# Kernel tuning notes

Hardware: AMD Instinct MI355X
Metric: run time of the kernel (lower is better)

Reference implementation:

```python
import jax, jax.numpy as jnp
import numpy as np

IN_V = 16
OUT_V = 16
HS = 64
INCR = 2
METRIC = jnp.array([1.0, -1.0, -1.0, -1.0], dtype=jnp.float32)


def setup_inputs() -> dict:
    key = jax.random.key(0)
    ks = jax.random.split(key, 9)
    B, N = 64, 1024
    vectors = jax.random.normal(ks[0], (B, N, IN_V, 4), dtype=jnp.float32)
    scalars = jax.random.normal(ks[1], (B, N, HS), dtype=jnp.float32)
    # kaiming-uniform-ish init scale for [out, in] weights
    def w(k, o, i):
        bound = 1.0 / np.sqrt(i)
        return jax.random.uniform(k, (o, i), jnp.float32, -bound, bound)
    Wq = w(ks[2], IN_V * INCR, IN_V)
    Wk = w(ks[3], IN_V * INCR, IN_V)
    Wv = w(ks[4], OUT_V, IN_V)  # exp() applied in forward (EquiLinearTimelike)
    Wq_s = w(ks[5], HS, HS)
    Wk_s = w(ks[6], HS, HS)
    bq_s = jax.random.uniform(ks[7], (HS,), jnp.float32, -1 / np.sqrt(HS), 1 / np.sqrt(HS))
    bk_s = jax.random.uniform(ks[8], (HS,), jnp.float32, -1 / np.sqrt(HS), 1 / np.sqrt(HS))
    return {"vectors": vectors, "scalars": scalars, "Wq": Wq, "Wq_s": Wq_s,
            "bq_s": bq_s, "Wk": Wk, "Wk_s": Wk_s, "bk_s": bk_s, "Wv": Wv}


def reference(vectors, scalars, Wq, Wq_s, bq_s, Wk, Wk_s, bk_s, Wv):
    B, N = vectors.shape[:2]
    # Lorentz squared norm: t^2 - x^2 - y^2 - z^2 over last axis -> [B,N,IN_V,1]
    norm = jnp.einsum('bnik,k->bni', vectors * vectors, METRIC)[..., None]
    vecs = vectors / jnp.sqrt(jnp.clip(jnp.abs(norm), 1e-5))
    # Q/K vector projections [B,N,IN_V*INCR,4] and scalar projections [B,N,HS]
    q_v = jnp.einsum('ij,bnjk->bnik', Wq, vecs)
    k_v = jnp.einsum('ij,bnjk->bnik', Wk, vecs)
    q_s = scalars @ Wq_s.T + bq_s
    k_s = scalars @ Wk_s.T + bk_s
    # embed: flatten vectors (K gets metric factor) and concat scalars
    q = jnp.concatenate([q_v.reshape(B, N, -1), q_s], axis=-1)
    k = jnp.concatenate([(k_v * METRIC).reshape(B, N, -1), k_s], axis=-1)
    # V: positive-weight (timelike) projection, flatten -> [B,N,OUT_V*4]
    v = jnp.einsum('ij,bnjk->bnik', jnp.exp(Wv), vecs).reshape(B, N, -1)
    # scaled dot-product attention over the particle axis
    scale = 1.0 / jnp.sqrt(jnp.asarray(q.shape[-1], q.dtype))
    scores = jnp.einsum('bqd,bkd->bqk', q, k) * scale
    attn = jax.nn.softmax(scores, axis=-1)
    out = jnp.einsum('bqk,bkd->bqd', attn, v)
    return out.reshape(B, N, -1, 4)
```

## Files before the change

kernel.cpp:

```cpp
#include <hip/hip_runtime.h>
#include <math.h>

typedef float f32x16 __attribute__((ext_vector_type(16)));
typedef short bf16x8 __attribute__((ext_vector_type(8)));
typedef short bf16x4 __attribute__((ext_vector_type(4)));
typedef unsigned short u16;
typedef unsigned int u32;

#define MFMA32(a, b, c) __builtin_amdgcn_mfma_f32_32x32x16_bf16(a, b, c, 0, 0, 0)

__device__ __forceinline__ u16 f2bf(float x) {
    u32 u = __float_as_uint(x);
    u += 0x7FFFu + ((u >> 16) & 1u);
    return (u16)(u >> 16);
}
__device__ __forceinline__ float bf2f(u16 h) {
    return __uint_as_float(((u32)h) << 16);
}
__device__ __forceinline__ void gload16(const void* g, void* l) {
    __builtin_amdgcn_global_load_lds(
        (const __attribute__((address_space(1))) unsigned int*)g,
        (__attribute__((address_space(3))) unsigned int*)l, 16, 0, 0);
}

__global__ __launch_bounds__(256) void g_kernel(
    const float* __restrict__ Wq, const float* __restrict__ Wk,
    const float* __restrict__ Wv,
    u16* __restrict__ gmh, u16* __restrict__ gml,
    u16* __restrict__ mvh, u16* __restrict__ mvl)
{
    const int bk = blockIdx.x;
    const int base = ((bk & 3) * 256 + threadIdx.x) * 4;
    if (bk < 4) {
#pragma unroll
        for (int i = 0; i < 4; ++i) {
            int e = base + i;
            int f = e >> 6, fp = e & 63;
            int c = f & 3, cp = fp & 3, j = f >> 2, jp = fp >> 2;
            float val = 0.f;
            if (c == cp) {
                float a0 = 0.f, a1 = 0.f;
#pragma unroll 8
                for (int ff = 0; ff < 32; ff += 2) {
                    a0 = fmaf(Wq[ff * 16 + j],       Wk[ff * 16 + jp],       a0);
                    a1 = fmaf(Wq[(ff + 1) * 16 + j], Wk[(ff + 1) * 16 + jp], a1);
                }
                val = (a0 + a1) * ((c == 0) ? 1.f : -1.f);
            }
            u16 h = f2bf(val);
            gmh[e] = h; gml[e] = f2bf(val - bf2f(h));
        }
    } else {
#pragma unroll
        for (int i = 0; i < 4; ++i) {
            int e = base + i;
            int f = e >> 6, fp = e & 63;
            float val = ((f & 3) == (fp & 3)) ? expf(Wv[(f >> 2) * 16 + (fp >> 2)]) : 0.f;
            u16 h = f2bf(val);
            mvh[e] = h; mvl[e] = f2bf(val - bf2f(h));
        }
    }
}

__global__ __launch_bounds__(256) void prep_kernel(
    const float* __restrict__ vectors, const float* __restrict__ scalars,
    const float* __restrict__ Wq_s, const float* __restrict__ bq_s,
    const float* __restrict__ Wk_s, const float* __restrict__ bk_s,
    const u16* __restrict__ gmh, const u16* __restrict__ gml,
    const u16* __restrict__ mvh, const u16* __restrict__ mvl,
    u16* __restrict__ qh, u16* __restrict__ ql,
    u16* __restrict__ kh, u16* __restrict__ kl,
    u16* __restrict__ vth)
{
    const int t = threadIdx.x;
    const int w = t >> 6;
    const int lane = t & 63;
    const int l31 = lane & 31, g = lane >> 5;
    const int b = blockIdx.x >> 5;
    const int n0 = (blockIdx.x & 31) << 5;
    const long tok0 = (long)b * 1024 + n0;
    const float SC2 = 0.07216878364870323f * 1.4426950408889634f;

    if (w == 1 || w == 2) {
        bf16x8 Ah[4], Al[4];
        const float* vrow = vectors + (tok0 + l31) * 64 + g * 8;
#pragma unroll
        for (int kk = 0; kk < 4; ++kk) {
            float4 x0 = *(const float4*)(vrow + kk * 16);
            float4 x1 = *(const float4*)(vrow + kk * 16 + 4);
            float nr0 = x0.x * x0.x - x0.y * x0.y - x0.z * x0.z - x0.w * x0.w;
            float iv0 = 1.0f / sqrtf(fmaxf(fabsf(nr0), 1e-5f));
            float nr1 = x1.x * x1.x - x1.y * x1.y - x1.z * x1.z - x1.w * x1.w;
            float iv1 = 1.0f / sqrtf(fmaxf(fabsf(nr1), 1e-5f));
            float xs[8] = {x0.x * iv0, x0.y * iv0, x0.z * iv0, x0.w * iv0,
                           x1.x * iv1, x1.y * iv1, x1.z * iv1, x1.w * iv1};
#pragma unroll
            for (int e = 0; e < 8; ++e) {
                u16 h = f2bf(xs[e]);
                Ah[kk][e] = (short)h;
                Al[kk][e] = (short)f2bf(xs[e] - bf2f(h));
            }
        }

        const u16* bhp = (w == 1) ? gmh : mvh;
        const u16* blp = (w == 1) ? gml : mvl;
#pragma unroll
        for (int tile = 0; tile < 2; ++tile) {
            const int fs = tile * 32 + l31;
            const u16* bh = bhp + fs * 64 + g * 8;
            const u16* bl = blp + fs * 64 + g * 8;
            f32x16 acc;
#pragma unroll
            for (int r = 0; r < 16; ++r) acc[r] = 0.f;
#pragma unroll
            for (int kk = 0; kk < 4; ++kk) {
                bf16x8 Bh = *(const bf16x8*)(bh + kk * 16);
                bf16x8 Bl = *(const bf16x8*)(bl + kk * 16);
                acc = MFMA32(Ah[kk], Bh, acc);
                acc = MFMA32(Al[kk], Bh, acc);
                acc = MFMA32(Ah[kk], Bl, acc);
            }
            if (w == 1) {
#pragma unroll
                for (int reg = 0; reg < 16; ++reg) {
                    int trow = (reg & 3) + 8 * (reg >> 2) + 4 * g;
                    float val = acc[reg];
                    u16 h = f2bf(val);
                    kh[(tok0 + trow) * 128 + fs] = h;
                    kl[(tok0 + trow) * 64 + fs] = f2bf(val - bf2f(h));
                }
            } else {
#pragma unroll
                for (int reg = 0; reg < 16; ++reg) {
                    int trow = (reg & 3) + 8 * (reg >> 2) + 4 * g;
                    vth[((long)b * 64 + fs) * 1024 + n0 + trow] = f2bf(acc[reg]);
                }
            }
        }
    } else {
        if (w == 0) {
            const float* vrow = vectors + (tok0 + l31) * 64 + g * 8;
#pragma unroll
            for (int kk = 0; kk < 4; ++kk) {
                float4 x0 = *(const float4*)(vrow + kk * 16);
                float4 x1 = *(const float4*)(vrow + kk * 16 + 4);
                float nr0 = x0.x * x0.x - x0.y * x0.y - x0.z * x0.z - x0.w * x0.w;
                float iv0 = SC2 / sqrtf(fmaxf(fabsf(nr0), 1e-5f));
                float nr1 = x1.x * x1.x - x1.y * x1.y - x1.z * x1.z - x1.w * x1.w;
                float iv1 = SC2 / sqrtf(fmaxf(fabsf(nr1), 1e-5f));
                float xs[8] = {x0.x * iv0, x0.y * iv0, x0.z * iv0, x0.w * iv0,
                               x1.x * iv1, x1.y * iv1, x1.z * iv1, x1.w * iv1};
                u16 hh[8], ll[8];
#pragma unroll
                for (int e = 0; e < 8; ++e) {
                    hh[e] = f2bf(xs[e]);
                    ll[e] = f2bf(xs[e] - bf2f(hh[e]));
                }
                *(int4*)(qh + (tok0 + l31) * 128 + kk * 16 + g * 8) = *(int4*)hh;
                *(int4*)(ql + (tok0 + l31) * 64 + kk * 16 + g * 8) = *(int4*)ll;
            }
        }
        const int isq = (w == 0);
        bf16x8 Ah[4];
        const float* xrow = scalars + (tok0 + l31) * 64 + g * 8;
#pragma unroll
        for (int kk = 0; kk < 4; ++kk) {
            float4 x0 = *(const float4*)(xrow + kk * 16);
            float4 x1 = *(const float4*)(xrow + kk * 16 + 4);
            float xs[8] = {x0.x, x0.y, x0.z, x0.w, x1.x, x1.y, x1.z, x1.w};
#pragma unroll
            for (int e = 0; e < 8; ++e) Ah[kk][e] = (short)f2bf(xs[e]);
        }
        const float sc = isq ? SC2 : 1.f;
        u16* oh = isq ? qh : kh;
#pragma unroll
        for (int ft = 0; ft < 2; ++ft) {
            const int fs = (ft << 5) + l31;
            const float* wrow = (isq ? Wq_s : Wk_s) + fs * 64 + g * 8;
            f32x16 acc;
#pragma unroll
            for (int r = 0; r < 16; ++r) acc[r] = 0.f;
#pragma unroll
            for (int kk = 0; kk < 4; ++kk) {
                float4 w0_ = *(const float4*)(wrow + kk * 16);
                float4 w1_ = *(const float4*)(wrow + kk * 16 + 4);
                float ws_[8] = {w0_.x, w0_.y, w0_.z, w0_.w, w1_.x, w1_.y, w1_.z, w1_.w};
                bf16x8 Bh;
#pragma unroll
                for (int e = 0; e < 8; ++e) Bh[e] = (short)f2bf(ws_[e]);
                acc = MFMA32(Ah[kk], Bh, acc);
            }
            const float bias = (isq ? bq_s : bk_s)[fs];
#pragma unroll
            for (int reg = 0; reg < 16; ++reg) {
                int trow = (reg & 3) + 8 * (reg >> 2) + 4 * g;
                oh[(tok0 + trow) * 128 + 64 + fs] = f2bf((acc[reg] + bias) * sc);
            }
        }
    }
}

__global__ __launch_bounds__(256) void attn_kernel(
    const u16* __restrict__ qh, const u16* __restrict__ ql,
    const u16* __restrict__ kh, const u16* __restrict__ kl,
    const u16* __restrict__ vth, u16* __restrict__ pob,
    float2* __restrict__ pml)
{
    __shared__ u16 KH[2 * 32 * 128];
    __shared__ u16 KL[2 * 32 * 64];
    __shared__ u16 VH[2 * 64 * 40];

    const int t = threadIdx.x;
    const int lane = t & 63;
    const int w = t >> 6;
    const int l31 = lane & 31, g = lane >> 5;

    const int bid = blockIdx.x;
    const int xcd = bid & 7;
    const int idx = bid >> 3;
    const int b = xcd * 8 + (idx >> 4);
    const int qt = (idx >> 1) & 7;
    const int half = idx & 1;
    const int kv0 = half << 9;

    const int qi = qt * 128 + w * 32 + l31;
    const long qtok = (long)b * 1024 + qi;

    bf16x8 Qh[8], Qlv[4];
    {
        const u16* qhp = qh + qtok * 128 + g * 8;
        const u16* qlp = ql + qtok * 64 + g * 8;
#pragma unroll
        for (int c = 0; c < 8; ++c) Qh[c] = *(const bf16x8*)(qhp + c * 16);
#pragma unroll
        for (int c = 0; c < 4; ++c) Qlv[c] = *(const bf16x8*)(qlp + c * 16);
    }

    const int r0 = 8 * w + (lane >> 4);
    const int r1 = r0 + 4;
    const int su0 = (lane & 15) ^ (r0 & 15);
    const int su1 = (lane & 15) ^ (r1 & 15);
    const u16* kh0 = kh + ((long)b * 1024 + kv0 + r0) * 128 + su0 * 8;
    const u16* kh1 = kh + ((long)b * 1024 + kv0 + r1) * 128 + su1 * 8;
    const int rl_ = 8 * w + (lane >> 3);
    const int sul = (lane & 7) ^ (rl_ & 7);
    const u16* kl0 = kl + ((long)b * 1024 + kv0 + rl_) * 64 + sul * 8;

    const int vdv = t >> 2, vq4 = t & 3;
    const u16* vhg = vth + ((long)b * 64 + vdv) * 1024 + kv0 + vq4 * 8;
    u16* vdst = VH + vdv * 40 + vq4 * 8;
    int4 rv0;

#define STAGEK(kt, bf) do { \
        gload16(kh0 + (long)(kt) * 128, KH + (bf) * 4096 + w * 1024); \
        gload16(kh1 + (long)(kt) * 128, KH + (bf) * 4096 + w * 1024 + 512); \
        gload16(kl0 + (long)(kt) * 64,  KL + (bf) * 2048 + w * 512); \
    } while (0)

    f32x16 o0, o1;
#pragma unroll
    for (int r = 0; r < 16; ++r) { o0[r] = 0.f; o1[r] = 0.f; }
    float m_run = -1e30f, l_run = 0.f;

    rv0 = *(const int4*)(vhg);
    STAGEK(0, 0);
    *(int4*)(vdst) = rv0;
    __syncthreads();

#pragma unroll 2
    for (int it = 0; it < 16; ++it) {
        const int cb = it & 1;
        if (it < 15) {
            rv0 = *(const int4*)(vhg + (it + 1) * 32);
            STAGEK((it + 1) * 32, cb ^ 1);
        }

        f32x16 sA, sB;
#pragma unroll
        for (int r = 0; r < 16; ++r) { sA[r] = 0.f; sB[r] = 0.f; }
        const u16* kbh = KH + cb * 4096 + l31 * 128;
        const u16* kbl = KL + cb * 2048 + l31 * 64;
        const int rs = l31 & 15, rs7 = l31 & 7;
        __builtin_amdgcn_s_setprio(1);
#pragma unroll
        for (int c = 0; c < 4; ++c) {
            bf16x8 fh = *(const bf16x8*)(kbh + ((g + 2 * c) ^ rs) * 8);
            bf16x8 fl = *(const bf16x8*)(kbl + ((g + 2 * c) ^ rs7) * 8);
            sA = MFMA32(fh, Qh[c], sA);
            sB = MFMA32(fl, Qh[c], sB);
            sB = MFMA32(fh, Qlv[c], sB);
        }
#pragma unroll
        for (int c = 4; c < 8; ++c) {
            bf16x8 fh = *(const bf16x8*)(kbh + ((g + 2 * c) ^ rs) * 8);
            sA = MFMA32(fh, Qh[c], sA);
        }
        __builtin_amdgcn_s_setprio(0);

        float s[16];
#pragma unroll
        for (int r = 0; r < 16; ++r) s[r] = sA[r] + sB[r];
        float m01 = fmaxf(s[0], s[1]),   m23 = fmaxf(s[2], s[3]);
        float m45 = fmaxf(s[4], s[5]),   m67 = fmaxf(s[6], s[7]);
        float m89 = fmaxf(s[8], s[9]),   mab = fmaxf(s[10], s[11]);
        float mcd = fmaxf(s[12], s[13]), mef = fmaxf(s[14], s[15]);
        float mt = fmaxf(fmaxf(fmaxf(m01, m23), fmaxf(m45, m67)),
                         fmaxf(fmaxf(m89, mab), fmaxf(mcd, mef)));
        mt = fmaxf(mt, __shfl_xor(mt, 32));
        if (!__all(mt - m_run <= 11.54f)) {
            float mn = fmaxf(m_run, mt);
            float corr = __builtin_amdgcn_exp2f(m_run - mn);
            l_run *= corr;
#pragma unroll
            for (int r = 0; r < 16; ++r) { o0[r] *= corr; o1[r] *= corr; }
            m_run = mn;
        }
#pragma unroll
        for (int r = 0; r < 16; ++r) s[r] = __builtin_amdgcn_exp2f(s[r] - m_run);
        float p01 = s[0] + s[1],   p23 = s[2] + s[3];
        float p45 = s[4] + s[5],   p67 = s[6] + s[7];
        float p89 = s[8] + s[9],   pab = s[10] + s[11];
        float pcd = s[12] + s[13], pef = s[14] + s[15];
        float ps = ((p01 + p23) + (p45 + p67)) + ((p89 + pab) + (pcd + pef));
        ps += __shfl_xor(ps, 32);
        l_run += ps;

        u32 pk[4], pk2[4];
#pragma unroll
        for (int e = 0; e < 4; ++e) {
            pk[e]  = __builtin_amdgcn_perm(__float_as_uint(s[2 * e + 1]),
                                           __float_as_uint(s[2 * e]), 0x07060302u);
            pk2[e] = __builtin_amdgcn_perm(__float_as_uint(s[8 + 2 * e + 1]),
                                           __float_as_uint(s[8 + 2 * e]), 0x07060302u);
        }
        bf16x8 ph0 = *(bf16x8*)pk;
        bf16x8 ph1 = *(bf16x8*)pk2;

        const u16* vb = VH + cb * 2560;
        bf16x8 v00, v01, v10, v11;
        {
            const u16* p00 = vb + l31 * 40 + g * 4;
            const u16* p10 = vb + (32 + l31) * 40 + g * 4;
            bf16x4 a0 = *(const bf16x4*)(p00);      bf16x4 a1 = *(const bf16x4*)(p00 + 8);
            bf16x4 b0 = *(const bf16x4*)(p00 + 16); bf16x4 b1 = *(const bf16x4*)(p00 + 24);
            bf16x4 c0 = *(const bf16x4*)(p10);      bf16x4 c1 = *(const bf16x4*)(p10 + 8);
            bf16x4 d0 = *(const bf16x4*)(p10 + 16); bf16x4 d1 = *(const bf16x4*)(p10 + 24);
            v00 = __builtin_shufflevector(a0, a1, 0, 1, 2, 3, 4, 5, 6, 7);
            v01 = __builtin_shufflevector(b0, b1, 0, 1, 2, 3, 4, 5, 6, 7);
            v10 = __builtin_shufflevector(c0, c1, 0, 1, 2, 3, 4, 5, 6, 7);
            v11 = __builtin_shufflevector(d0, d1, 0, 1, 2, 3, 4, 5, 6, 7);
        }

        __builtin_amdgcn_s_setprio(1);
        o0 = MFMA32(v00, ph0, o0);
        o0 = MFMA32(v01, ph1, o0);
        o1 = MFMA32(v10, ph0, o1);
        o1 = MFMA32(v11, ph1, o1);
        __builtin_amdgcn_s_setprio(0);

        if (it < 15) *(int4*)(vdst + (cb ^ 1) * 2560) = rv0;
        __syncthreads();
    }

    u16* poA = pob + (long)half * 4194304 + qtok * 64;
#pragma unroll
    for (int sg = 0; sg < 4; ++sg) {
        u32 pk0 = (u32)f2bf(o0[4 * sg + 0]) | ((u32)f2bf(o0[4 * sg + 1]) << 16);
        u32 pk1 = (u32)f2bf(o0[4 * sg + 2]) | ((u32)f2bf(o0[4 * sg + 3]) << 16);
        *(int2*)(poA + sg * 8 + g * 4) = make_int2((int)pk0, (int)pk1);
        u32 pk2_ = (u32)f2bf(o1[4 * sg + 0]) | ((u32)f2bf(o1[4 * sg + 1]) << 16);
        u32 pk3_ = (u32)f2bf(o1[4 * sg + 2]) | ((u32)f2bf(o1[4 * sg + 3]) << 16);
        *(int2*)(poA + 32 + sg * 8 + g * 4) = make_int2((int)pk2_, (int)pk3_);
    }
    if (g == 0) {
        pml[((long)half * 64 + b) * 1024 + qi] = make_float2(m_run, l_run);
    }
#undef STAGEK
}

__global__ __launch_bounds__(256) void merge_kernel(
    const u16* __restrict__ pob, const float2* __restrict__ pml,
    float* __restrict__ out)
{
    const int idx = blockIdx.x * 256 + threadIdx.x;
    const int q = idx >> 2;
    const int part = idx & 3;
    float2 a = pml[q];
    float2 c = pml[65536 + q];
    float m = fmaxf(a.x, c.x);
    float w0 = __builtin_amdgcn_exp2f(a.x - m), w1 = __builtin_amdgcn_exp2f(c.x - m);
    float inv = 1.0f / (w0 * a.y + w1 * c.y);
    const u16* p0 = pob + (long)q * 64 + part * 16;
    const u16* p1 = p0 + 4194304;
    u16 va[16], vb[16];
    *(int4*)&va[0] = *(const int4*)p0;
    *(int4*)&va[8] = *(const int4*)(p0 + 8);
    *(int4*)&vb[0] = *(const int4*)p1;
    *(int4*)&vb[8] = *(const int4*)(p1 + 8);
    float4* op = (float4*)(out + (long)q * 64 + part * 16);
#pragma unroll
    for (int j = 0; j < 4; ++j) {
        float4 o4;
        o4.x = (w0 * bf2f(va[j * 4 + 0]) + w1 * bf2f(vb[j * 4 + 0])) * inv;
        o4.y = (w0 * bf2f(va[j * 4 + 1]) + w1 * bf2f(vb[j * 4 + 1])) * inv;
        o4.z = (w0 * bf2f(va[j * 4 + 2]) + w1 * bf2f(vb[j * 4 + 2])) * inv;
        o4.w = (w0 * bf2f(va[j * 4 + 3]) + w1 * bf2f(vb[j * 4 + 3])) * inv;
        op[j] = o4;
    }
}

extern "C" void kernel_launch(void* const* d_in, const int* in_sizes, int n_in,
                              void* d_out, int out_size, void* d_ws, size_t ws_size,
                              hipStream_t stream) {
    const float* vectors = (const float*)d_in[0];
    const float* scalars = (const float*)d_in[1];
    const float* Wq   = (const float*)d_in[2];
    const float* Wq_s = (const float*)d_in[3];
    const float* bq_s = (const float*)d_in[4];
    const float* Wk   = (const float*)d_in[5];
    const float* Wk_s = (const float*)d_in[6];
    const float* bk_s = (const float*)d_in[7];
    const float* Wv   = (const float*)d_in[8];
    float* o = (float*)d_out;

    u16* qh  = (u16*)d_ws;
    u16* ql  = qh + 8388608;
    u16* kh  = ql + 4194304;
    u16* kl  = kh + 8388608;
    u16* vth = kl + 4194304;
    u16* pob = vth + 4194304;
    float2* pml = (float2*)(pob + 8388608);
    u16* gmh = (u16*)(pml + 131072);
    u16* gml = gmh + 4096;
    u16* mvh = gml + 4096;
    u16* mvl = mvh + 4096;

    g_kernel<<<8, 256, 0, stream>>>(Wq, Wk, Wv, gmh, gml, mvh, mvl);
    prep_kernel<<<2048, 256, 0, stream>>>(vectors, scalars, Wq_s, bq_s,
                                          Wk_s, bk_s, gmh, gml, mvh, mvl,
                                          qh, ql, kh, kl, vth);
    attn_kernel<<<1024, 256, 0, stream>>>(qh, ql, kh, kl, vth, pob, pml);
    merge_kernel<<<1024, 256, 0, stream>>>(pob, pml, o);
}
```

Measured before the change: 103.7 us.

## Deepen K staging to four LDS buffers and load V straight to registers

K/KL staging moves from double to quadruple LDS buffering with a prefetch distance of two tiles. The V tile is no longer staged through LDS; each wave loads its MFMA operands directly from global memory at the top of each iteration. Barriers drop to every other iteration. The aim is to cut LDS round-trips and barrier stalls, at the cost of each of the four waves fetching the same V data from L2 and exposing more global-load latency inside the loop.

```diff
diff --git a/kernel.cpp b/kernel.cpp
--- a/kernel.cpp
+++ b/kernel.cpp
@@ -206,9 +206,8 @@
     const u16* __restrict__ vth, u16* __restrict__ pob,
     float2* __restrict__ pml)
 {
-    __shared__ u16 KH[2 * 32 * 128];
-    __shared__ u16 KL[2 * 32 * 64];
-    __shared__ u16 VH[2 * 64 * 40];
+    __shared__ u16 KH[4 * 32 * 128];
+    __shared__ u16 KL[4 * 32 * 64];
 
     const int t = threadIdx.x;
     const int lane = t & 63;
@@ -246,10 +245,8 @@
     const int sul = (lane & 7) ^ (rl_ & 7);
     const u16* kl0 = kl + ((long)b * 1024 + kv0 + rl_) * 64 + sul * 8;
 
-    const int vdv = t >> 2, vq4 = t & 3;
-    const u16* vhg = vth + ((long)b * 64 + vdv) * 1024 + kv0 + vq4 * 8;
-    u16* vdst = VH + vdv * 40 + vq4 * 8;
-    int4 rv0;
+    const u16* vgA = vth + ((long)b * 64 + l31) * 1024 + kv0 + g * 4;
+    const u16* vgB = vgA + 32 * 1024;
 
 #define STAGEK(kt, bf) do { \
         gload16(kh0 + (long)(kt) * 128, KH + (bf) * 4096 + w * 1024); \
@@ -262,18 +259,21 @@
     for (int r = 0; r < 16; ++r) { o0[r] = 0.f; o1[r] = 0.f; }
     float m_run = -1e30f, l_run = 0.f;
 
-    rv0 = *(const int4*)(vhg);
     STAGEK(0, 0);
-    *(int4*)(vdst) = rv0;
+    STAGEK(32, 1);
     __syncthreads();
 
-#pragma unroll 2
+#pragma unroll 4
     for (int it = 0; it < 16; ++it) {
-        const int cb = it & 1;
-        if (it < 15) {
-            rv0 = *(const int4*)(vhg + (it + 1) * 32);
-            STAGEK((it + 1) * 32, cb ^ 1);
-        }
+        const int cb = it & 3;
+        if (it < 14) STAGEK((it + 2) * 32, (it + 2) & 3);
+
+        const u16* vA = vgA + it * 32;
+        const u16* vB = vgB + it * 32;
+        bf16x4 a0 = *(const bf16x4*)(vA);      bf16x4 a1 = *(const bf16x4*)(vA + 8);
+        bf16x4 b0 = *(const bf16x4*)(vA + 16); bf16x4 b1 = *(const bf16x4*)(vA + 24);
+        bf16x4 c0 = *(const bf16x4*)(vB);      bf16x4 c1 = *(const bf16x4*)(vB + 8);
+        bf16x4 d0 = *(const bf16x4*)(vB + 16); bf16x4 d1 = *(const bf16x4*)(vB + 24);
 
         f32x16 sA, sB;
 #pragma unroll
@@ -336,20 +336,10 @@
         bf16x8 ph0 = *(bf16x8*)pk;
         bf16x8 ph1 = *(bf16x8*)pk2;
 
-        const u16* vb = VH + cb * 2560;
-        bf16x8 v00, v01, v10, v11;
-        {
-            const u16* p00 = vb + l31 * 40 + g * 4;
-            const u16* p10 = vb + (32 + l31) * 40 + g * 4;
-            bf16x4 a0 = *(const bf16x4*)(p00);      bf16x4 a1 = *(const bf16x4*)(p00 + 8);
-            bf16x4 b0 = *(const bf16x4*)(p00 + 16); bf16x4 b1 = *(const bf16x4*)(p00 + 24);
-            bf16x4 c0 = *(const bf16x4*)(p10);      bf16x4 c1 = *(const bf16x4*)(p10 + 8);
-            bf16x4 d0 = *(const bf16x4*)(p10 + 16); bf16x4 d1 = *(const bf16x4*)(p10 + 24);
-            v00 = __builtin_shufflevector(a0, a1, 0, 1, 2, 3, 4, 5, 6, 7);
-            v01 = __builtin_shufflevector(b0, b1, 0, 1, 2, 3, 4, 5, 6, 7);
-            v10 = __builtin_shufflevector(c0, c1, 0, 1, 2, 3, 4, 5, 6, 7);
-            v11 = __builtin_shufflevector(d0, d1, 0, 1, 2, 3, 4, 5, 6, 7);
-        }
+        bf16x8 v00 = __builtin_shufflevector(a0, a1, 0, 1, 2, 3, 4, 5, 6, 7);
+        bf16x8 v01 = __builtin_shufflevector(b0, b1, 0, 1, 2, 3, 4, 5, 6, 7);
+        bf16x8 v10 = __builtin_shufflevector(c0, c1, 0, 1, 2, 3, 4, 5, 6, 7);
+        bf16x8 v11 = __builtin_shufflevector(d0, d1, 0, 1, 2, 3, 4, 5, 6, 7);
 
         __builtin_amdgcn_s_setprio(1);
         o0 = MFMA32(v00, ph0, o0);
@@ -358,8 +348,7 @@
         o1 = MFMA32(v11, ph1, o1);
         __builtin_amdgcn_s_setprio(0);
 
-        if (it < 15) *(int4*)(vdst + (cb ^ 1) * 2560) = rv0;
-        __syncthreads();
+        if (it & 1) __syncthreads();
     }
 
     u16* poA = pob + (long)half * 4194304 + qtok * 64;
```

Result: slower. 125.6 us (+21.1%).

## Drop split-KV partials and merge kernel; process full key range per block

Applied to the files above, without the earlier changes.

Each attention block now iterates over all 1024 keys instead of half, normalizes by the running sum, and writes fp32 output directly. This removes the partial-output/stat buffers, the bf16 round trip, and the separate merge kernel launch. In exchange the grid is halved, so fewer blocks are resident per CU and latency hiding for the attention loop may drop.

```diff
diff --git a/kernel.cpp b/kernel.cpp
--- a/kernel.cpp
+++ b/kernel.cpp
@@ -203,8 +203,7 @@
 __global__ __launch_bounds__(256) void attn_kernel(
     const u16* __restrict__ qh, const u16* __restrict__ ql,
     const u16* __restrict__ kh, const u16* __restrict__ kl,
-    const u16* __restrict__ vth, u16* __restrict__ pob,
-    float2* __restrict__ pml)
+    const u16* __restrict__ vth, float* __restrict__ out)
 {
     __shared__ u16 KH[2 * 32 * 128];
     __shared__ u16 KL[2 * 32 * 64];
@@ -216,12 +215,8 @@
     const int l31 = lane & 31, g = lane >> 5;
 
     const int bid = blockIdx.x;
-    const int xcd = bid & 7;
-    const int idx = bid >> 3;
-    const int b = xcd * 8 + (idx >> 4);
-    const int qt = (idx >> 1) & 7;
-    const int half = idx & 1;
-    const int kv0 = half << 9;
+    const int b = ((bid & 7) << 3) + (bid >> 6);
+    const int qt = (bid >> 3) & 7;
 
     const int qi = qt * 128 + w * 32 + l31;
     const long qtok = (long)b * 1024 + qi;
@@ -240,14 +235,14 @@
     const int r1 = r0 + 4;
     const int su0 = (lane & 15) ^ (r0 & 15);
     const int su1 = (lane & 15) ^ (r1 & 15);
-    const u16* kh0 = kh + ((long)b * 1024 + kv0 + r0) * 128 + su0 * 8;
-    const u16* kh1 = kh + ((long)b * 1024 + kv0 + r1) * 128 + su1 * 8;
+    const u16* kh0 = kh + ((long)b * 1024 + r0) * 128 + su0 * 8;
+    const u16* kh1 = kh + ((long)b * 1024 + r1) * 128 + su1 * 8;
     const int rl_ = 8 * w + (lane >> 3);
     const int sul = (lane & 7) ^ (rl_ & 7);
-    const u16* kl0 = kl + ((long)b * 1024 + kv0 + rl_) * 64 + sul * 8;
+    const u16* kl0 = kl + ((long)b * 1024 + rl_) * 64 + sul * 8;
 
     const int vdv = t >> 2, vq4 = t & 3;
-    const u16* vhg = vth + ((long)b * 64 + vdv) * 1024 + kv0 + vq4 * 8;
+    const u16* vhg = vth + ((long)b * 64 + vdv) * 1024 + vq4 * 8;
     u16* vdst = VH + vdv * 40 + vq4 * 8;
     int4 rv0;
 
@@ -268,9 +263,9 @@
     __syncthreads();
 
 #pragma unroll 2
-    for (int it = 0; it < 16; ++it) {
+    for (int it = 0; it < 32; ++it) {
         const int cb = it & 1;
-        if (it < 15) {
+        if (it < 31) {
             rv0 = *(const int4*)(vhg + (it + 1) * 32);
             STAGEK((it + 1) * 32, cb ^ 1);
         }
@@ -358,55 +353,20 @@
         o1 = MFMA32(v11, ph1, o1);
         __builtin_amdgcn_s_setprio(0);
 
-        if (it < 15) *(int4*)(vdst + (cb ^ 1) * 2560) = rv0;
+        if (it < 31) *(int4*)(vdst + (cb ^ 1) * 2560) = rv0;
         __syncthreads();
     }
 
-    u16* poA = pob + (long)half * 4194304 + qtok * 64;
+    float inv = 1.0f / l_run;
+    float* op = out + qtok * 64;
 #pragma unroll
     for (int sg = 0; sg < 4; ++sg) {
-        u32 pk0 = (u32)f2bf(o0[4 * sg + 0]) | ((u32)f2bf(o0[4 * sg + 1]) << 16);
-        u32 pk1 = (u32)f2bf(o0[4 * sg + 2]) | ((u32)f2bf(o0[4 * sg + 3]) << 16);
-        *(int2*)(poA + sg * 8 + g * 4) = make_int2((int)pk0, (int)pk1);
-        u32 pk2_ = (u32)f2bf(o1[4 * sg + 0]) | ((u32)f2bf(o1[4 * sg + 1]) << 16);
-        u32 pk3_ = (u32)f2bf(o1[4 * sg + 2]) | ((u32)f2bf(o1[4 * sg + 3]) << 16);
-        *(int2*)(poA + 32 + sg * 8 + g * 4) = make_int2((int)pk2_, (int)pk3_);
-    }
-    if (g == 0) {
-        pml[((long)half * 64 + b) * 1024 + qi] = make_float2(m_run, l_run);
+        *(float4*)(op + sg * 8 + g * 4) = make_float4(
+            o0[4*sg+0]*inv, o0[4*sg+1]*inv, o0[4*sg+2]*inv, o0[4*sg+3]*inv);
+        *(float4*)(op + 32 + sg * 8 + g * 4) = make_float4(
+            o1[4*sg+0]*inv, o1[4*sg+1]*inv, o1[4*sg+2]*inv, o1[4*sg+3]*inv);
     }
 #undef STAGEK
-}
-
-__global__ __launch_bounds__(256) void merge_kernel(
-    const u16* __restrict__ pob, const float2* __restrict__ pml,
-    float* __restrict__ out)
-{
-    const int idx = blockIdx.x * 256 + threadIdx.x;
-    const int q = idx >> 2;
-    const int part = idx & 3;
-    float2 a = pml[q];
-    float2 c = pml[65536 + q];
-    float m = fmaxf(a.x, c.x);
-    float w0 = __builtin_amdgcn_exp2f(a.x - m), w1 = __builtin_amdgcn_exp2f(c.x - m);
-    float inv = 1.0f / (w0 * a.y + w1 * c.y);
-    const u16* p0 = pob + (long)q * 64 + part * 16;
-    const u16* p1 = p0 + 4194304;
-    u16 va[16], vb[16];
-    *(int4*)&va[0] = *(const int4*)p0;
-    *(int4*)&va[8] = *(const int4*)(p0 + 8);
-    *(int4*)&vb[0] = *(const int4*)p1;
-    *(int4*)&vb[8] = *(const int4*)(p1 + 8);
-    float4* op = (float4*)(out + (long)q * 64 + part * 16);
-#pragma unroll
-    for (int j = 0; j < 4; ++j) {
-        float4 o4;
-        o4.x = (w0 * bf2f(va[j * 4 + 0]) + w1 * bf2f(vb[j * 4 + 0])) * inv;
-        o4.y = (w0 * bf2f(va[j * 4 + 1]) + w1 * bf2f(vb[j * 4 + 1])) * inv;
-        o4.z = (w0 * bf2f(va[j * 4 + 2]) + w1 * bf2f(vb[j * 4 + 2])) * inv;
-        o4.w = (w0 * bf2f(va[j * 4 + 3]) + w1 * bf2f(vb[j * 4 + 3])) * inv;
-        op[j] = o4;
-    }
 }
 
 extern "C" void kernel_launch(void* const* d_in, const int* in_sizes, int n_in,
@@ -428,9 +388,7 @@
     u16* kh  = ql + 4194304;
     u16* kl  = kh + 8388608;
     u16* vth = kl + 4194304;
-    u16* pob = vth + 4194304;
-    float2* pml = (float2*)(pob + 8388608);
-    u16* gmh = (u16*)(pml + 131072);
+    u16* gmh = vth + 4194304;
     u16* gml = gmh + 4096;
     u16* mvh = gml + 4096;
     u16* mvl = mvh + 4096;
@@ -439,6 +397,5 @@
     prep_kernel<<<2048, 256, 0, stream>>>(vectors, scalars, Wq_s, bq_s,
                                           Wk_s, bk_s, gmh, gml, mvh, mvl,
                                           qh, ql, kh, kl, vth);
-    attn_kernel<<<1024, 256, 0, stream>>>(qh, ql, kh, kl, vth, pob, pml);
-    merge_kernel<<<1024, 256, 0, stream>>>(pob, pml, o);
-}
+    attn_kernel<<<512, 256, 0, stream>>>(qh, ql, kh, kl, vth, o);
+}
```

Measured after the change: 92.55 us (median of 3 runs). -10.8%, faster.
